# Performance work log

Measured on AMD Instinct MI355X. Metric: run time of the kernel, lower is better.

Reference implementation:

```python
import jax, jax.numpy as jnp
import numpy as np

N_SRC, N_DST, K, T = 16384, 8192, 16, 2
NODE_IN, EDGE_IN, TIME_D = 128, 64, 128
D_MODEL = NODE_IN + TIME_D + EDGE_IN  # 320
N_HEAD, D_K = 8, 64                   # d_k = d_v
HID = 128
LN_EPS = 1e-5


def setup_inputs() -> dict:
    key = jax.random.key(0)
    ks = jax.random.split(key, 10)
    std_qk = np.sqrt(2.0 / (D_MODEL + D_K)).astype(np.float32)
    return {
        "node_features": jax.random.normal(ks[0], (N_SRC, NODE_IN), jnp.float32),
        "edge_features": jax.random.normal(ks[1], (N_DST, K, T, EDGE_IN), jnp.float32),
        "delta_t": jax.random.uniform(ks[2], (N_DST, K, T), jnp.float32) * 100.0,
        "neigh_idx": jax.random.randint(ks[3], (N_DST, K), 0, N_SRC),
        "basis_freq": jnp.asarray(1.0 / 10 ** np.linspace(0, 9, TIME_D), jnp.float32),
        "phase": jnp.zeros((TIME_D,), jnp.float32),
        "w_qs": jax.random.normal(ks[4], (N_HEAD * D_K, D_MODEL), jnp.float32) * std_qk,
        "w_ks": jax.random.normal(ks[5], (N_HEAD * D_K, D_MODEL), jnp.float32) * std_qk,
        "w_vs": jax.random.normal(ks[6], (N_HEAD * D_K, D_MODEL), jnp.float32) * std_qk,
        "fc_w": jax.random.normal(ks[7], (D_MODEL, N_HEAD * D_K), jnp.float32) * 0.03,
        "fc_b": jnp.zeros((D_MODEL,), jnp.float32),
        "ln_g": jnp.ones((D_MODEL,), jnp.float32),
        "ln_b": jnp.zeros((D_MODEL,), jnp.float32),
        "node_w": jax.random.normal(ks[8], (HID, 2 * NODE_IN + TIME_D + EDGE_IN), jnp.float32) * 0.05,
        "node_b": jnp.zeros((HID,), jnp.float32),
    }


def reference(node_features, edge_features, delta_t, neigh_idx, basis_freq, phase,
              w_qs, w_ks, w_vs, fc_w, fc_b, ln_g, ln_b, node_w, node_b):
    h_dst = node_features[:N_DST]                                  # [N, NODE_IN]
    # message_func: per-edge time encoding + gather src feats + concat
    te = jnp.cos(delta_t[..., None] * basis_freq + phase)          # [N, K, T, TIME_D]
    h_nb = node_features[neigh_idx]                                # [N, K, NODE_IN] (irregular gather)
    h_nb = jnp.broadcast_to(h_nb[:, :, None, :], (N_DST, K, T, NODE_IN))
    m = jnp.concatenate([h_nb, edge_features, te], axis=-1)        # [N, K, T, D_MODEL]
    m = m.reshape(N_DST, K * T, D_MODEL)                           # mailbox kv
    # reduce_func query: [h_dst, zeros(edge_in), time_encode(0)=cos(phase)]
    t0 = jnp.broadcast_to(jnp.cos(phase), (N_DST, TIME_D))
    q = jnp.concatenate([h_dst, jnp.zeros((N_DST, EDGE_IN), h_dst.dtype), t0], axis=-1)  # [N, D_MODEL]
    # multi-head attention (len_q = 1)
    qh = (q @ w_qs.T).reshape(N_DST, N_HEAD, D_K)
    kh = (m @ w_ks.T).reshape(N_DST, K * T, N_HEAD, D_K)
    vh = (m @ w_vs.T).reshape(N_DST, K * T, N_HEAD, D_K)
    scores = jnp.einsum('nhd,nlhd->nhl', qh, kh) / np.float32(np.sqrt(D_K))
    attn = jax.nn.softmax(scores, axis=-1)
    ctx = jnp.einsum('nhl,nlhd->nhd', attn, vh).reshape(N_DST, N_HEAD * D_K)
    out = ctx @ fc_w.T + fc_b
    x = out + q                                                    # residual
    mu = x.mean(-1, keepdims=True)
    var = x.var(-1, keepdims=True)
    h_neigh = ln_g * (x - mu) * jax.lax.rsqrt(var + LN_EPS) + ln_b  # layer norm
    h = jnp.concatenate([h_dst, h_neigh], axis=-1)                 # [N, 2*NODE_IN+TIME_D+EDGE_IN]
    return jax.nn.relu(h @ node_w.T + node_b)                      # [N, HID]
```

## Files before the change

### kernel.cpp

```cpp
#include <hip/hip_runtime.h>
#include <math.h>

#define LNB      32
#define NODE_IN  128
#define EDGE_IN  64
#define TIME_D   128
#define D_MODEL  320
#define N_HEAD   8
#define D_K      64
#define NHD      512
#define HID      128
#define IN2      448
#define N_DSTN   8192

typedef __attribute__((ext_vector_type(8))) short bf16x8;
typedef __attribute__((ext_vector_type(4))) float f32x4;
#define MFMA16(a,b,c) __builtin_amdgcn_mfma_f32_16x16x32_bf16(a,b,c,0,0,0)

#define WS_QKM   0
#define WS_WQK   20971520
#define WS_WVF   21299200
#define WS_NWC   22118400
#define WS_F32   22175744
#define WS_X     22182784

#define F_C0     0
#define F_C0K    512
#define F_CC     3072
#define F_B2     3392

__device__ __forceinline__ unsigned short f2bf(float f) {
  __bf16 h = (__bf16)f;
  return __builtin_bit_cast(unsigned short, h);
}
__device__ __forceinline__ bf16x8 pack8(const float* v) {
  unsigned short b8[8];
  #pragma unroll
  for (int j = 0; j < 8; ++j) b8[j] = f2bf(v[j]);
  return *(const bf16x8*)b8;
}

#define GLDS(srcp, dstp) __builtin_amdgcn_global_load_lds(                     \
    (const __attribute__((address_space(1))) unsigned int*)(const void*)(srcp),\
    (__attribute__((address_space(3))) unsigned int*)(void*)(dstp), 16, 0, 0)

__global__ __launch_bounds__(256)
void prep1a(const float* __restrict__ nw, const float* __restrict__ lng,
            const float* __restrict__ fcb, const float* __restrict__ ph,
            unsigned short* __restrict__ ws)
{
  int i = blockIdx.x * 256 + threadIdx.x;
  unsigned short* nwc = ws + WS_NWC;
  float* f32r = (float*)(ws + WS_F32);
  if (i < 16384) {
    int o = i >> 7, k = i & 127;
    nwc[o * IN2 + k] = f2bf(nw[(size_t)o * IN2 + k]);
  } else if (i < 57344) {
    int j = i - 16384, o = j / 320, c = j - o * 320;
    nwc[o * IN2 + 128 + c] = f2bf(nw[(size_t)o * IN2 + 128 + c] * lng[c]);
  } else if (i < 57664) {
    int c = i - 57344;
    f32r[F_CC + c] = fcb[c] + (c >= 192 ? __cosf(ph[c - 192]) : 0.f);
  }
}

__global__ __launch_bounds__(256)
void prep1b(const float* __restrict__ wq, const float* __restrict__ ph,
            const float* __restrict__ nw, const float* __restrict__ lnb_,
            const float* __restrict__ nb, unsigned short* __restrict__ ws)
{
  float* f32r = (float*)(ws + WS_F32);
  int gw = (blockIdx.x * 256 + threadIdx.x) >> 6;
  int ln = threadIdx.x & 63;
  if (gw < 512) {
    float s = __cosf(ph[ln])      * wq[(size_t)gw * D_MODEL + 192 + ln]
            + __cosf(ph[ln + 64]) * wq[(size_t)gw * D_MODEL + 256 + ln];
    #pragma unroll
    for (int off = 32; off >= 1; off >>= 1) s += __shfl_xor(s, off);
    if (ln == 0) f32r[F_C0 + gw] = s;
  } else {
    int o = gw - 512;
    float s = 0.f;
    #pragma unroll
    for (int k = 0; k < 5; ++k) {
      int c = ln + 64 * k;
      s += nw[(size_t)o * IN2 + 128 + c] * lnb_[c];
    }
    #pragma unroll
    for (int off = 32; off >= 1; off >>= 1) s += __shfl_xor(s, off);
    if (ln == 0) f32r[F_B2 + o] = nb[o] + s;
  }
}

__global__ __launch_bounds__(256)
void prep_c0k(const float* __restrict__ wk, unsigned short* __restrict__ ws)
{
  float* f32r = (float*)(ws + WS_F32);
  int gw = (blockIdx.x * 256 + threadIdx.x) >> 6;
  int ln = threadIdx.x & 63;
  int h = gw / 320, d = gw - h * 320;
  float s = f32r[F_C0 + h * 64 + ln] * wk[(size_t)(h * 64 + ln) * D_MODEL + d];
  #pragma unroll
  for (int off = 32; off >= 1; off >>= 1) s += __shfl_xor(s, off);
  if (ln == 0) f32r[F_C0K + gw] = s;
}

__global__ __launch_bounds__(256)
void prep_wqk(const float* __restrict__ wq, const float* __restrict__ wk,
              unsigned short* __restrict__ ws)
{
  __shared__ float sQw[64 * 128];
  __shared__ float sKw[64 * 32];
  int h = blockIdx.x / 10, d0 = (blockIdx.x - h * 10) * 32;
  int tid = threadIdx.x;
  #pragma unroll 4
  for (int it = 0; it < 32; ++it) {
    int idx = it * 256 + tid;
    int r = idx >> 7, c = idx & 127;
    sQw[idx] = wq[(size_t)(h * 64 + r) * D_MODEL + c];
  }
  #pragma unroll
  for (int it = 0; it < 8; ++it) {
    int idx = it * 256 + tid;
    int r = idx >> 5, c = idx & 31;
    sKw[idx] = wk[(size_t)(h * 64 + r) * D_MODEL + d0 + c];
  }
  __syncthreads();
  int di = tid >> 3, k0 = (tid & 7) * 16;
  float acc[16] = {};
  for (int dk = 0; dk < 64; ++dk) {
    float w = sKw[dk * 32 + di];
    #pragma unroll
    for (int j = 0; j < 16; ++j) acc[j] += w * sQw[dk * 128 + k0 + j];
  }
  unsigned short* dst = ws + WS_WQK + (size_t)(h * 320 + d0 + di) * 128 + k0;
  #pragma unroll
  for (int j = 0; j < 16; ++j) dst[j] = f2bf(acc[j]);
}

__global__ __launch_bounds__(256)
void prep_wvf(const float* __restrict__ fcw, const float* __restrict__ wv,
              unsigned short* __restrict__ ws)
{
  __shared__ float sF[32 * 64];
  __shared__ float sW[64 * 32];
  int b = blockIdx.x;
  int h = b / 100, r2 = b - h * 100;
  int ct = r2 / 10;
  int c0 = ct * 32, d0 = (r2 - ct * 10) * 32;
  int tid = threadIdx.x;
  #pragma unroll
  for (int it = 0; it < 8; ++it) {
    int idx = it * 256 + tid;
    int i = idx >> 6, jj = idx & 63;
    sF[idx] = fcw[(size_t)(c0 + i) * NHD + h * 64 + jj];
  }
  #pragma unroll
  for (int it = 0; it < 8; ++it) {
    int idx = it * 256 + tid;
    int jj = idx >> 5, i = idx & 31;
    sW[idx] = wv[(size_t)(h * 64 + jj) * D_MODEL + d0 + i];
  }
  __syncthreads();
  int ci = tid >> 3, dj0 = (tid & 7) * 4;
  float acc[4] = {};
  for (int jj = 0; jj < 64; ++jj) {
    float f = sF[ci * 64 + jj];
    #pragma unroll
    for (int k = 0; k < 4; ++k) acc[k] += f * sW[jj * 32 + dj0 + k];
  }
  unsigned short* wvf = ws + WS_WVF;
  #pragma unroll
  for (int k = 0; k < 4; ++k)
    wvf[(size_t)(c0 + ci) * 2560 + (size_t)(d0 + dj0 + k) * 8 + h] = f2bf(acc[k]);
}

__global__ __launch_bounds__(256, 6)
void tgat_qk(const float* __restrict__ nf, const unsigned short* __restrict__ ws,
             unsigned short* __restrict__ qkm)
{
  __shared__ alignas(16) unsigned short sA[64 * 136];
  const int tid = threadIdx.x, wid = tid >> 6, lane = tid & 63, qd = lane >> 4, lm = lane & 15;
  const int mt_blk = blockIdx.x / 20, nt_blk = blockIdx.x - mt_blk * 20;
  const int n0 = mt_blk * 64, c0 = nt_blk * 128;
  const unsigned short* wqk = ws + WS_WQK;
  const float* f32r = (const float*)(ws + WS_F32);

  {
    int n = tid >> 2, k0 = (tid & 3) * 32;
    const float4* src = (const float4*)(nf + (size_t)(n0 + n) * NODE_IN + k0);
    #pragma unroll
    for (int q = 0; q < 4; ++q) {
      float4 f0 = src[2 * q], f1 = src[2 * q + 1];
      float v[8] = {f0.x, f0.y, f0.z, f0.w, f1.x, f1.y, f1.z, f1.w};
      *(bf16x8*)&sA[n * 136 + k0 + q * 8] = pack8(v);
    }
  }
  __syncthreads();

  f32x4 acc[2][4] = {};
  for (int kt = 0; kt < 4; ++kt) {
    bf16x8 a[4];
    #pragma unroll
    for (int mt = 0; mt < 4; ++mt)
      a[mt] = *(const bf16x8*)&sA[(mt * 16 + lm) * 136 + kt * 32 + qd * 8];
    #pragma unroll
    for (int t = 0; t < 2; ++t) {
      int cg = c0 + (2 * wid + t) * 16 + lm;
      bf16x8 b = *(const bf16x8*)&wqk[(size_t)cg * 128 + kt * 32 + qd * 8];
      #pragma unroll
      for (int mt = 0; mt < 4; ++mt) acc[t][mt] = MFMA16(a[mt], b, acc[t][mt]);
    }
  }
  #pragma unroll
  for (int t = 0; t < 2; ++t) {
    int cg = c0 + (2 * wid + t) * 16 + lm;
    float ck = f32r[F_C0K + cg];
    #pragma unroll
    for (int mt = 0; mt < 4; ++mt)
      #pragma unroll
      for (int r = 0; r < 4; ++r)
        qkm[(size_t)(n0 + mt * 16 + qd * 4 + r) * 2560 + cg] = f2bf(acc[t][mt][r] + ck);
  }
}

__global__ __launch_bounds__(256, 6)
void tgat_attn(const float* __restrict__ nf, const float* __restrict__ ef,
               const float* __restrict__ dtp, const int* __restrict__ nidx,
               const float* __restrict__ freq, const float* __restrict__ ph,
               unsigned short* __restrict__ qkm)
{
  __shared__ alignas(16) unsigned short sM[LNB * 328];
  __shared__ alignas(16) unsigned short sATT[16 * 40];

  const int tid = threadIdx.x;
  const int wid = tid >> 6, lane = tid & 63, qd = lane >> 4, lm = lane & 15;
  const int n = blockIdx.x;
  unsigned short* qn = qkm + (size_t)n * 2560;

  #pragma unroll 1
  for (int it = 0; it < 5; ++it) {
    int g = it * 256 + tid;
    int l = g & 31, dg = g >> 5;
    int d0 = dg * 8;
    float v[8];
    if (dg < 16) {
      int ni = nidx[n * 16 + (l >> 1)];
      const float4* src = (const float4*)(nf + (size_t)ni * NODE_IN + d0);
      float4 f0 = src[0], f1 = src[1];
      v[0]=f0.x; v[1]=f0.y; v[2]=f0.z; v[3]=f0.w; v[4]=f1.x; v[5]=f1.y; v[6]=f1.z; v[7]=f1.w;
    } else if (dg < 24) {
      const float4* src = (const float4*)(ef + ((size_t)n * LNB + l) * EDGE_IN + (d0 - NODE_IN));
      float4 f0 = src[0], f1 = src[1];
      v[0]=f0.x; v[1]=f0.y; v[2]=f0.z; v[3]=f0.w; v[4]=f1.x; v[5]=f1.y; v[6]=f1.z; v[7]=f1.w;
    } else {
      int dd = d0 - 192;
      float dt = dtp[(size_t)n * LNB + l];
      const float4* fq = (const float4*)(freq + dd);
      const float4* pp = (const float4*)(ph + dd);
      float4 q0 = fq[0], q1 = fq[1], p0 = pp[0], p1 = pp[1];
      v[0] = __cosf(dt * q0.x + p0.x); v[1] = __cosf(dt * q0.y + p0.y);
      v[2] = __cosf(dt * q0.z + p0.z); v[3] = __cosf(dt * q0.w + p0.w);
      v[4] = __cosf(dt * q1.x + p1.x); v[5] = __cosf(dt * q1.y + p1.y);
      v[6] = __cosf(dt * q1.z + p1.z); v[7] = __cosf(dt * q1.w + p1.w);
    }
    *(bf16x8*)&sM[l * 328 + d0] = pack8(v);
  }

  bf16x8 qfrag[10];
  if (wid == 0) {
    #pragma unroll
    for (int kt = 0; kt < 10; ++kt) {
      qfrag[kt] = (bf16x8){0,0,0,0,0,0,0,0};
      if (lm < 8) qfrag[kt] = *(const bf16x8*)&qn[lm * 320 + kt * 32 + qd * 8];
    }
  }
  __syncthreads();

  const int tbeg = (wid == 0) ? 0 : 2 + (wid - 1) * 6;
  const int tcnt = (wid == 0) ? 2 : 6;
  bf16x8 afr[6];

  if (wid == 0) {
    f32x4 acc0 = {}, acc1 = {};
    #pragma unroll
    for (int kt = 0; kt < 10; ++kt) {
      bf16x8 a0 = *(const bf16x8*)&sM[lm * 328 + kt * 32 + qd * 8];
      bf16x8 a1 = *(const bf16x8*)&sM[(16 + lm) * 328 + kt * 32 + qd * 8];
      acc0 = MFMA16(a0, qfrag[kt], acc0);
      acc1 = MFMA16(a1, qfrag[kt], acc1);
    }
    float s[8], e[8];
    #pragma unroll
    for (int r = 0; r < 4; ++r) { s[r] = acc0[r] * 0.125f; s[4 + r] = acc1[r] * 0.125f; }
    float mx = s[0];
    #pragma unroll
    for (int i = 1; i < 8; ++i) mx = fmaxf(mx, s[i]);
    mx = fmaxf(mx, __shfl_xor(mx, 16));
    mx = fmaxf(mx, __shfl_xor(mx, 32));
    float sum = 0.f;
    #pragma unroll
    for (int i = 0; i < 8; ++i) { e[i] = __expf(s[i] - mx); sum += e[i]; }
    sum += __shfl_xor(sum, 16);
    sum += __shfl_xor(sum, 32);
    float inv = 1.f / sum;
    #pragma unroll
    for (int i = 0; i < 8; ++i) {
      int l = (i < 4) ? (qd * 4 + i) : (16 + qd * 4 + (i - 4));
      sATT[lm * 40 + l] = f2bf(e[i] * inv);
    }
  } else {
    #pragma unroll
    for (int u = 0; u < 6; ++u) {
      int d = (tbeg + u) * 16 + lm;
      unsigned short a8[8];
      #pragma unroll
      for (int j = 0; j < 8; ++j) a8[j] = sM[(qd * 8 + j) * 328 + d];
      afr[u] = *(const bf16x8*)a8;
    }
  }
  __syncthreads();

  if (wid == 0) {
    #pragma unroll
    for (int u = 0; u < 2; ++u) {
      int d = u * 16 + lm;
      unsigned short a8[8];
      #pragma unroll
      for (int j = 0; j < 8; ++j) a8[j] = sM[(qd * 8 + j) * 328 + d];
      afr[u] = *(const bf16x8*)a8;
    }
  }
  bf16x8 batt = *(const bf16x8*)&sATT[lm * 40 + qd * 8];
  #pragma unroll
  for (int u = 0; u < 6; ++u) {
    if (u < tcnt) {
      int dtile = tbeg + u;
      f32x4 acc = {};
      acc = MFMA16(afr[u], batt, acc);
      if (lm < 8) {
        #pragma unroll
        for (int r = 0; r < 4; ++r)
          qn[(dtile * 16 + qd * 4 + r) * 8 + lm] = f2bf(acc[r]);
      }
    }
  }
}

__global__ __launch_bounds__(512, 1)
void tgat_xgemm(const unsigned short* __restrict__ ws,
                const unsigned short* __restrict__ qkm, float* __restrict__ xacc)
{
  __shared__ alignas(16) unsigned short sA[2][128 * 128];
  __shared__ alignas(16) unsigned short sB[2][80 * 128];
  const int tid = threadIdx.x, wid = tid >> 6, lane = tid & 63;
  const int qd = lane >> 4, lm = lane & 15;
  const int xcd = blockIdx.x & 7, j = blockIdx.x >> 3;
  const int nb = j & 3, mb = xcd + 8 * (j >> 2);
  const int n0 = mb * 128, c0 = nb * 80;
  const unsigned short* wvf = ws + WS_WVF;

  const int rhi = lane >> 4, blo = lane & 15;

  #define STAGE(kc, buf) {                                                     \
    for (int ri = wid; ri < 52; ri += 8) {                                     \
      if (ri < 32) {                                                           \
        int r = ri * 4 + rhi;                                                  \
        int blk = blo ^ (r & 7);                                               \
        GLDS(qkm + (size_t)(n0 + r) * 2560 + (kc) * 128 + blk * 8,             \
             &sA[buf][ri * 512]);                                              \
      } else {                                                                 \
        int jb = ri - 32;                                                      \
        int r = jb * 4 + rhi;                                                  \
        int blk = blo ^ (r & 7);                                               \
        GLDS(wvf + (size_t)(c0 + r) * 2560 + (kc) * 128 + blk * 8,             \
             &sB[buf][jb * 512]);                                              \
      }                                                                        \
    } }

  f32x4 acc[5] = {};
  STAGE(0, 0);
  __syncthreads();

  for (int c = 0; c < 20; ++c) {
    if (c < 19) STAGE(c + 1, (c + 1) & 1);
    const unsigned short* Ab = sA[c & 1];
    const unsigned short* Bb = sB[c & 1];
    const int s = lm & 7;
    #pragma unroll
    for (int kt = 0; kt < 4; ++kt) {
      const int blk = ((kt << 2) | qd) ^ s;
      bf16x8 a = *(const bf16x8*)&Ab[(wid * 16 + lm) * 128 + blk * 8];
      #pragma unroll
      for (int u = 0; u < 5; ++u) {
        bf16x8 b = *(const bf16x8*)&Bb[(u * 16 + lm) * 128 + blk * 8];
        acc[u] = MFMA16(a, b, acc[u]);
      }
    }
    __syncthreads();
  }

  #pragma unroll
  for (int u = 0; u < 5; ++u)
    #pragma unroll
    for (int r = 0; r < 4; ++r)
      xacc[(size_t)(n0 + wid * 16 + qd * 4 + r) * 320 + c0 + u * 16 + lm] = acc[u][r];
  #undef STAGE
}

__global__ __launch_bounds__(256, 4)
void tgat_post2(const float* __restrict__ nf, const unsigned short* __restrict__ ws,
                const float* __restrict__ xacc, float* __restrict__ out)
{
  __shared__ alignas(16) unsigned short sQb[16 * 136];
  __shared__ alignas(16) unsigned short sXb[16 * 328];
  const int tid = threadIdx.x, wid = tid >> 6, lane = tid & 63, qd = lane >> 4, lm = lane & 15;
  const int n0 = blockIdx.x * 16;
  const unsigned short* nwc = ws + WS_NWC;
  const float* f32r = (const float*)(ws + WS_F32);

  {
    int nn = tid >> 4, kk = (tid & 15) * 8;
    const float4* src = (const float4*)(nf + (size_t)(n0 + nn) * NODE_IN + kk);
    float4 f0 = src[0], f1 = src[1];
    float v8[8] = {f0.x, f0.y, f0.z, f0.w, f1.x, f1.y, f1.z, f1.w};
    *(bf16x8*)&sQb[nn * 136 + kk] = pack8(v8);
  }
  const int rr = tid >> 4, cl = tid & 15;
  float v[20], s1 = 0.f, s2 = 0.f;
  #pragma unroll
  for (int u = 0; u < 20; ++u) {
    int c = u * 16 + cl;
    float x = xacc[(size_t)(n0 + rr) * 320 + c] + f32r[F_CC + c];
    if (c < 128) x += nf[(size_t)(n0 + rr) * NODE_IN + c];
    v[u] = x; s1 += x; s2 += x * x;
  }
  #pragma unroll
  for (int off = 8; off >= 1; off >>= 1) { s1 += __shfl_xor(s1, off); s2 += __shfl_xor(s2, off); }
  float mean = s1 * (1.f / D_MODEL);
  float var  = s2 * (1.f / D_MODEL) - mean * mean;
  float rstd = rsqrtf(var + 1e-5f);
  #pragma unroll
  for (int u = 0; u < 20; ++u) {
    int c = u * 16 + cl;
    sXb[rr * 328 + c] = f2bf((v[u] - mean) * rstd);
  }
  __syncthreads();

  #pragma unroll
  for (int t = 0; t < 2; ++t) {
    int o = (wid * 2 + t) * 16 + lm;
    f32x4 acc = {};
    for (int kt = 0; kt < 14; ++kt) {
      bf16x8 a;
      if (kt < 4) a = *(const bf16x8*)&sQb[lm * 136 + kt * 32 + qd * 8];
      else        a = *(const bf16x8*)&sXb[lm * 328 + (kt - 4) * 32 + qd * 8];
      bf16x8 b = *(const bf16x8*)&nwc[(size_t)o * IN2 + kt * 32 + qd * 8];
      acc = MFMA16(a, b, acc);
    }
    float bz = f32r[F_B2 + o];
    #pragma unroll
    for (int r = 0; r < 4; ++r)
      out[(size_t)(n0 + qd * 4 + r) * HID + o] = fmaxf(acc[r] + bz, 0.f);
  }
}

extern "C" void kernel_launch(void* const* d_in, const int* in_sizes, int n_in,
                              void* d_out, int out_size, void* d_ws, size_t ws_size,
                              hipStream_t stream) {
  const float* nf   = (const float*)d_in[0];
  const float* ef   = (const float*)d_in[1];
  const float* dtp  = (const float*)d_in[2];
  const int*   nidx = (const int*)  d_in[3];
  const float* freq = (const float*)d_in[4];
  const float* ph   = (const float*)d_in[5];
  const float* wq   = (const float*)d_in[6];
  const float* wk   = (const float*)d_in[7];
  const float* wv   = (const float*)d_in[8];
  const float* fcw  = (const float*)d_in[9];
  const float* fcb  = (const float*)d_in[10];
  const float* lng  = (const float*)d_in[11];
  const float* lnb_ = (const float*)d_in[12];
  const float* nw   = (const float*)d_in[13];
  const float* nb   = (const float*)d_in[14];
  float* out = (float*)d_out;
  unsigned short* ws = (unsigned short*)d_ws;
  unsigned short* qkm = ws + WS_QKM;
  float* xacc = (float*)(ws + WS_X);

  prep1a  <<<226, 256, 0, stream>>>(nw, lng, fcb, ph, ws);
  prep1b  <<<160, 256, 0, stream>>>(wq, ph, nw, lnb_, nb, ws);
  prep_c0k<<<640, 256, 0, stream>>>(wk, ws);
  prep_wqk<<<80,  256, 0, stream>>>(wq, wk, ws);
  prep_wvf<<<800, 256, 0, stream>>>(fcw, wv, ws);
  tgat_qk   <<<2560, 256, 0, stream>>>(nf, ws, qkm);
  tgat_attn <<<8192, 256, 0, stream>>>(nf, ef, dtp, nidx, freq, ph, qkm);
  tgat_xgemm<<<256,  512, 0, stream>>>(ws, qkm, xacc);
  tgat_post2<<<512,  256, 0, stream>>>(nf, ws, xacc, out);
}
```

Measured before the change: 253.8 us.

## Merge prep kernels and overlap attention scoring with mailbox staging

Four weight-preparation kernels are merged into one launch that dispatches on block index, cutting launch overhead and serialization gaps. In the attention kernel, wave 0 now computes the scores by loading gathered features, edge features and time encodings straight from global memory into MFMA fragments. Meanwhile the other three waves fill the shared mailbox tile, so scoring and softmax no longer wait on a block-wide barrier. The final attention-times-V tiles are redistributed evenly across all four waves. Occupancy is lowered to 5 blocks per SIMD, and wave 0 now duplicates global loads.

```diff
diff --git a/kernel.cpp b/kernel.cpp
--- a/kernel.cpp
+++ b/kernel.cpp
@@ -45,50 +45,110 @@
     (__attribute__((address_space(3))) unsigned int*)(void*)(dstp), 16, 0, 0)
 
 __global__ __launch_bounds__(256)
-void prep1a(const float* __restrict__ nw, const float* __restrict__ lng,
-            const float* __restrict__ fcb, const float* __restrict__ ph,
-            unsigned short* __restrict__ ws)
+void prep_all(const float* __restrict__ nw, const float* __restrict__ lng,
+              const float* __restrict__ fcb, const float* __restrict__ ph,
+              const float* __restrict__ wq, const float* __restrict__ lnb_,
+              const float* __restrict__ nb, const float* __restrict__ wk,
+              const float* __restrict__ fcw, const float* __restrict__ wv,
+              unsigned short* __restrict__ ws)
 {
-  int i = blockIdx.x * 256 + threadIdx.x;
+  __shared__ float smem[10240];
+  const int b = blockIdx.x, tid = threadIdx.x;
   unsigned short* nwc = ws + WS_NWC;
   float* f32r = (float*)(ws + WS_F32);
-  if (i < 16384) {
-    int o = i >> 7, k = i & 127;
-    nwc[o * IN2 + k] = f2bf(nw[(size_t)o * IN2 + k]);
-  } else if (i < 57344) {
-    int j = i - 16384, o = j / 320, c = j - o * 320;
-    nwc[o * IN2 + 128 + c] = f2bf(nw[(size_t)o * IN2 + 128 + c] * lng[c]);
-  } else if (i < 57664) {
-    int c = i - 57344;
-    f32r[F_CC + c] = fcb[c] + (c >= 192 ? __cosf(ph[c - 192]) : 0.f);
-  }
-}
-
-__global__ __launch_bounds__(256)
-void prep1b(const float* __restrict__ wq, const float* __restrict__ ph,
-            const float* __restrict__ nw, const float* __restrict__ lnb_,
-            const float* __restrict__ nb, unsigned short* __restrict__ ws)
-{
-  float* f32r = (float*)(ws + WS_F32);
-  int gw = (blockIdx.x * 256 + threadIdx.x) >> 6;
-  int ln = threadIdx.x & 63;
-  if (gw < 512) {
-    float s = __cosf(ph[ln])      * wq[(size_t)gw * D_MODEL + 192 + ln]
-            + __cosf(ph[ln + 64]) * wq[(size_t)gw * D_MODEL + 256 + ln];
-    #pragma unroll
-    for (int off = 32; off >= 1; off >>= 1) s += __shfl_xor(s, off);
-    if (ln == 0) f32r[F_C0 + gw] = s;
+
+  if (b < 226) {
+    int i = b * 256 + tid;
+    if (i < 16384) {
+      int o = i >> 7, k = i & 127;
+      nwc[o * IN2 + k] = f2bf(nw[(size_t)o * IN2 + k]);
+    } else if (i < 57344) {
+      int j = i - 16384, o = j / 320, c = j - o * 320;
+      nwc[o * IN2 + 128 + c] = f2bf(nw[(size_t)o * IN2 + 128 + c] * lng[c]);
+    } else if (i < 57664) {
+      int c = i - 57344;
+      f32r[F_CC + c] = fcb[c] + (c >= 192 ? __cosf(ph[c - 192]) : 0.f);
+    }
+  } else if (b < 386) {
+    int gw = ((b - 226) * 256 + tid) >> 6;
+    int ln = tid & 63;
+    if (gw < 512) {
+      float s = __cosf(ph[ln])      * wq[(size_t)gw * D_MODEL + 192 + ln]
+              + __cosf(ph[ln + 64]) * wq[(size_t)gw * D_MODEL + 256 + ln];
+      #pragma unroll
+      for (int off = 32; off >= 1; off >>= 1) s += __shfl_xor(s, off);
+      if (ln == 0) f32r[F_C0 + gw] = s;
+    } else {
+      int o = gw - 512;
+      float s = 0.f;
+      #pragma unroll
+      for (int k = 0; k < 5; ++k) {
+        int c = ln + 64 * k;
+        s += nw[(size_t)o * IN2 + 128 + c] * lnb_[c];
+      }
+      #pragma unroll
+      for (int off = 32; off >= 1; off >>= 1) s += __shfl_xor(s, off);
+      if (ln == 0) f32r[F_B2 + o] = nb[o] + s;
+    }
+  } else if (b < 466) {
+    float* sQw = smem;
+    float* sKw = smem + 8192;
+    int bw = b - 386;
+    int h = bw / 10, d0 = (bw - h * 10) * 32;
+    #pragma unroll 4
+    for (int it = 0; it < 32; ++it) {
+      int idx = it * 256 + tid;
+      int r = idx >> 7, c = idx & 127;
+      sQw[idx] = wq[(size_t)(h * 64 + r) * D_MODEL + c];
+    }
+    #pragma unroll
+    for (int it = 0; it < 8; ++it) {
+      int idx = it * 256 + tid;
+      int r = idx >> 5, c = idx & 31;
+      sKw[idx] = wk[(size_t)(h * 64 + r) * D_MODEL + d0 + c];
+    }
+    __syncthreads();
+    int di = tid >> 3, k0 = (tid & 7) * 16;
+    float acc[16] = {};
+    for (int dk = 0; dk < 64; ++dk) {
+      float w = sKw[dk * 32 + di];
+      #pragma unroll
+      for (int j = 0; j < 16; ++j) acc[j] += w * sQw[dk * 128 + k0 + j];
+    }
+    unsigned short* dst = ws + WS_WQK + (size_t)(h * 320 + d0 + di) * 128 + k0;
+    #pragma unroll
+    for (int j = 0; j < 16; ++j) dst[j] = f2bf(acc[j]);
   } else {
-    int o = gw - 512;
-    float s = 0.f;
-    #pragma unroll
-    for (int k = 0; k < 5; ++k) {
-      int c = ln + 64 * k;
-      s += nw[(size_t)o * IN2 + 128 + c] * lnb_[c];
-    }
-    #pragma unroll
-    for (int off = 32; off >= 1; off >>= 1) s += __shfl_xor(s, off);
-    if (ln == 0) f32r[F_B2 + o] = nb[o] + s;
+    float* sF = smem;
+    float* sW = smem + 2048;
+    int bb = b - 466;
+    int h = bb / 100, r2 = bb - h * 100;
+    int ct = r2 / 10;
+    int c0 = ct * 32, d0 = (r2 - ct * 10) * 32;
+    #pragma unroll
+    for (int it = 0; it < 8; ++it) {
+      int idx = it * 256 + tid;
+      int i = idx >> 6, jj = idx & 63;
+      sF[idx] = fcw[(size_t)(c0 + i) * NHD + h * 64 + jj];
+    }
+    #pragma unroll
+    for (int it = 0; it < 8; ++it) {
+      int idx = it * 256 + tid;
+      int jj = idx >> 5, i = idx & 31;
+      sW[idx] = wv[(size_t)(h * 64 + jj) * D_MODEL + d0 + i];
+    }
+    __syncthreads();
+    int ci = tid >> 3, dj0 = (tid & 7) * 4;
+    float acc[4] = {};
+    for (int jj = 0; jj < 64; ++jj) {
+      float f = sF[ci * 64 + jj];
+      #pragma unroll
+      for (int k = 0; k < 4; ++k) acc[k] += f * sW[jj * 32 + dj0 + k];
+    }
+    unsigned short* wvf = ws + WS_WVF;
+    #pragma unroll
+    for (int k = 0; k < 4; ++k)
+      wvf[(size_t)(c0 + ci) * 2560 + (size_t)(d0 + dj0 + k) * 8 + h] = f2bf(acc[k]);
   }
 }
 
@@ -103,76 +163,6 @@
   #pragma unroll
   for (int off = 32; off >= 1; off >>= 1) s += __shfl_xor(s, off);
   if (ln == 0) f32r[F_C0K + gw] = s;
-}
-
-__global__ __launch_bounds__(256)
-void prep_wqk(const float* __restrict__ wq, const float* __restrict__ wk,
-              unsigned short* __restrict__ ws)
-{
-  __shared__ float sQw[64 * 128];
-  __shared__ float sKw[64 * 32];
-  int h = blockIdx.x / 10, d0 = (blockIdx.x - h * 10) * 32;
-  int tid = threadIdx.x;
-  #pragma unroll 4
-  for (int it = 0; it < 32; ++it) {
-    int idx = it * 256 + tid;
-    int r = idx >> 7, c = idx & 127;
-    sQw[idx] = wq[(size_t)(h * 64 + r) * D_MODEL + c];
-  }
-  #pragma unroll
-  for (int it = 0; it < 8; ++it) {
-    int idx = it * 256 + tid;
-    int r = idx >> 5, c = idx & 31;
-    sKw[idx] = wk[(size_t)(h * 64 + r) * D_MODEL + d0 + c];
-  }
-  __syncthreads();
-  int di = tid >> 3, k0 = (tid & 7) * 16;
-  float acc[16] = {};
-  for (int dk = 0; dk < 64; ++dk) {
-    float w = sKw[dk * 32 + di];
-    #pragma unroll
-    for (int j = 0; j < 16; ++j) acc[j] += w * sQw[dk * 128 + k0 + j];
-  }
-  unsigned short* dst = ws + WS_WQK + (size_t)(h * 320 + d0 + di) * 128 + k0;
-  #pragma unroll
-  for (int j = 0; j < 16; ++j) dst[j] = f2bf(acc[j]);
-}
-
-__global__ __launch_bounds__(256)
-void prep_wvf(const float* __restrict__ fcw, const float* __restrict__ wv,
-              unsigned short* __restrict__ ws)
-{
-  __shared__ float sF[32 * 64];
-  __shared__ float sW[64 * 32];
-  int b = blockIdx.x;
-  int h = b / 100, r2 = b - h * 100;
-  int ct = r2 / 10;
-  int c0 = ct * 32, d0 = (r2 - ct * 10) * 32;
-  int tid = threadIdx.x;
-  #pragma unroll
-  for (int it = 0; it < 8; ++it) {
-    int idx = it * 256 + tid;
-    int i = idx >> 6, jj = idx & 63;
-    sF[idx] = fcw[(size_t)(c0 + i) * NHD + h * 64 + jj];
-  }
-  #pragma unroll
-  for (int it = 0; it < 8; ++it) {
-    int idx = it * 256 + tid;
-    int jj = idx >> 5, i = idx & 31;
-    sW[idx] = wv[(size_t)(h * 64 + jj) * D_MODEL + d0 + i];
-  }
-  __syncthreads();
-  int ci = tid >> 3, dj0 = (tid & 7) * 4;
-  float acc[4] = {};
-  for (int jj = 0; jj < 64; ++jj) {
-    float f = sF[ci * 64 + jj];
-    #pragma unroll
-    for (int k = 0; k < 4; ++k) acc[k] += f * sW[jj * 32 + dj0 + k];
-  }
-  unsigned short* wvf = ws + WS_WVF;
-  #pragma unroll
-  for (int k = 0; k < 4; ++k)
-    wvf[(size_t)(c0 + ci) * 2560 + (size_t)(d0 + dj0 + k) * 8 + h] = f2bf(acc[k]);
 }
 
 __global__ __launch_bounds__(256, 6)
@@ -224,7 +214,7 @@
   }
 }
 
-__global__ __launch_bounds__(256, 6)
+__global__ __launch_bounds__(256, 5)
 void tgat_attn(const float* __restrict__ nf, const float* __restrict__ ef,
                const float* __restrict__ dtp, const int* __restrict__ nidx,
                const float* __restrict__ freq, const float* __restrict__ ph,
@@ -238,57 +228,56 @@
   const int n = blockIdx.x;
   unsigned short* qn = qkm + (size_t)n * 2560;
 
-  #pragma unroll 1
-  for (int it = 0; it < 5; ++it) {
-    int g = it * 256 + tid;
-    int l = g & 31, dg = g >> 5;
-    int d0 = dg * 8;
-    float v[8];
-    if (dg < 16) {
-      int ni = nidx[n * 16 + (l >> 1)];
-      const float4* src = (const float4*)(nf + (size_t)ni * NODE_IN + d0);
-      float4 f0 = src[0], f1 = src[1];
-      v[0]=f0.x; v[1]=f0.y; v[2]=f0.z; v[3]=f0.w; v[4]=f1.x; v[5]=f1.y; v[6]=f1.z; v[7]=f1.w;
-    } else if (dg < 24) {
-      const float4* src = (const float4*)(ef + ((size_t)n * LNB + l) * EDGE_IN + (d0 - NODE_IN));
-      float4 f0 = src[0], f1 = src[1];
-      v[0]=f0.x; v[1]=f0.y; v[2]=f0.z; v[3]=f0.w; v[4]=f1.x; v[5]=f1.y; v[6]=f1.z; v[7]=f1.w;
-    } else {
-      int dd = d0 - 192;
-      float dt = dtp[(size_t)n * LNB + l];
+  if (wid == 0) {
+    const int ni0 = nidx[n * 16 + (lm >> 1)];
+    const int ni1 = nidx[n * 16 + 8 + (lm >> 1)];
+    const float dt0 = dtp[(size_t)n * LNB + lm];
+    const float dt1 = dtp[(size_t)n * LNB + 16 + lm];
+    f32x4 acc0 = {}, acc1 = {};
+    #pragma unroll
+    for (int kt = 0; kt < 4; ++kt) {
+      bf16x8 qf = (bf16x8){0,0,0,0,0,0,0,0};
+      if (lm < 8) qf = *(const bf16x8*)&qn[lm * 320 + kt * 32 + qd * 8];
+      const int d0 = kt * 32 + qd * 8;
+      const float4* s0 = (const float4*)(nf + (size_t)ni0 * NODE_IN + d0);
+      const float4* s1 = (const float4*)(nf + (size_t)ni1 * NODE_IN + d0);
+      float4 a = s0[0], b = s0[1], c = s1[0], d = s1[1];
+      float v0[8] = {a.x,a.y,a.z,a.w,b.x,b.y,b.z,b.w};
+      float v1[8] = {c.x,c.y,c.z,c.w,d.x,d.y,d.z,d.w};
+      acc0 = MFMA16(pack8(v0), qf, acc0);
+      acc1 = MFMA16(pack8(v1), qf, acc1);
+    }
+    #pragma unroll
+    for (int kt = 4; kt < 6; ++kt) {
+      bf16x8 qf = (bf16x8){0,0,0,0,0,0,0,0};
+      if (lm < 8) qf = *(const bf16x8*)&qn[lm * 320 + kt * 32 + qd * 8];
+      const int e0 = kt * 32 + qd * 8 - 128;
+      const float4* s0 = (const float4*)(ef + ((size_t)n * LNB + lm) * EDGE_IN + e0);
+      const float4* s1 = (const float4*)(ef + ((size_t)n * LNB + 16 + lm) * EDGE_IN + e0);
+      float4 a = s0[0], b = s0[1], c = s1[0], d = s1[1];
+      float v0[8] = {a.x,a.y,a.z,a.w,b.x,b.y,b.z,b.w};
+      float v1[8] = {c.x,c.y,c.z,c.w,d.x,d.y,d.z,d.w};
+      acc0 = MFMA16(pack8(v0), qf, acc0);
+      acc1 = MFMA16(pack8(v1), qf, acc1);
+    }
+    #pragma unroll
+    for (int kt = 6; kt < 10; ++kt) {
+      bf16x8 qf = (bf16x8){0,0,0,0,0,0,0,0};
+      if (lm < 8) qf = *(const bf16x8*)&qn[lm * 320 + kt * 32 + qd * 8];
+      const int dd = kt * 32 + qd * 8 - 192;
       const float4* fq = (const float4*)(freq + dd);
       const float4* pp = (const float4*)(ph + dd);
-      float4 q0 = fq[0], q1 = fq[1], p0 = pp[0], p1 = pp[1];
-      v[0] = __cosf(dt * q0.x + p0.x); v[1] = __cosf(dt * q0.y + p0.y);
-      v[2] = __cosf(dt * q0.z + p0.z); v[3] = __cosf(dt * q0.w + p0.w);
-      v[4] = __cosf(dt * q1.x + p1.x); v[5] = __cosf(dt * q1.y + p1.y);
-      v[6] = __cosf(dt * q1.z + p1.z); v[7] = __cosf(dt * q1.w + p1.w);
-    }
-    *(bf16x8*)&sM[l * 328 + d0] = pack8(v);
-  }
-
-  bf16x8 qfrag[10];
-  if (wid == 0) {
-    #pragma unroll
-    for (int kt = 0; kt < 10; ++kt) {
-      qfrag[kt] = (bf16x8){0,0,0,0,0,0,0,0};
-      if (lm < 8) qfrag[kt] = *(const bf16x8*)&qn[lm * 320 + kt * 32 + qd * 8];
-    }
-  }
-  __syncthreads();
-
-  const int tbeg = (wid == 0) ? 0 : 2 + (wid - 1) * 6;
-  const int tcnt = (wid == 0) ? 2 : 6;
-  bf16x8 afr[6];
-
-  if (wid == 0) {
-    f32x4 acc0 = {}, acc1 = {};
-    #pragma unroll
-    for (int kt = 0; kt < 10; ++kt) {
-      bf16x8 a0 = *(const bf16x8*)&sM[lm * 328 + kt * 32 + qd * 8];
-      bf16x8 a1 = *(const bf16x8*)&sM[(16 + lm) * 328 + kt * 32 + qd * 8];
-      acc0 = MFMA16(a0, qfrag[kt], acc0);
-      acc1 = MFMA16(a1, qfrag[kt], acc1);
+      float4 f0 = fq[0], f1 = fq[1], p0 = pp[0], p1 = pp[1];
+      float v0[8] = {__cosf(dt0*f0.x+p0.x), __cosf(dt0*f0.y+p0.y),
+                     __cosf(dt0*f0.z+p0.z), __cosf(dt0*f0.w+p0.w),
+                     __cosf(dt0*f1.x+p1.x), __cosf(dt0*f1.y+p1.y),
+                     __cosf(dt0*f1.z+p1.z), __cosf(dt0*f1.w+p1.w)};
+      float v1[8] = {__cosf(dt1*f0.x+p0.x), __cosf(dt1*f0.y+p0.y),
+                     __cosf(dt1*f0.z+p0.z), __cosf(dt1*f0.w+p0.w),
+                     __cosf(dt1*f1.x+p1.x), __cosf(dt1*f1.y+p1.y),
+                     __cosf(dt1*f1.z+p1.z), __cosf(dt1*f1.w+p1.w)};
+      acc0 = MFMA16(pack8(v0), qf, acc0);
+      acc1 = MFMA16(pack8(v1), qf, acc1);
     }
     float s[8], e[8];
     #pragma unroll
@@ -310,39 +299,54 @@
       sATT[lm * 40 + l] = f2bf(e[i] * inv);
     }
   } else {
-    #pragma unroll
-    for (int u = 0; u < 6; ++u) {
-      int d = (tbeg + u) * 16 + lm;
-      unsigned short a8[8];
-      #pragma unroll
-      for (int j = 0; j < 8; ++j) a8[j] = sM[(qd * 8 + j) * 328 + d];
-      afr[u] = *(const bf16x8*)a8;
+    const int t3 = tid - 64;
+    #pragma unroll 1
+    for (int it = 0; it < 7; ++it) {
+      int g = it * 192 + t3;
+      if (g < 1280) {
+        int l = g & 31, dg = g >> 5;
+        int d0 = dg * 8;
+        float v[8];
+        if (dg < 16) {
+          int ni = nidx[n * 16 + (l >> 1)];
+          const float4* src = (const float4*)(nf + (size_t)ni * NODE_IN + d0);
+          float4 f0 = src[0], f1 = src[1];
+          v[0]=f0.x; v[1]=f0.y; v[2]=f0.z; v[3]=f0.w; v[4]=f1.x; v[5]=f1.y; v[6]=f1.z; v[7]=f1.w;
+        } else if (dg < 24) {
+          const float4* src = (const float4*)(ef + ((size_t)n * LNB + l) * EDGE_IN + (d0 - NODE_IN));
+          float4 f0 = src[0], f1 = src[1];
+          v[0]=f0.x; v[1]=f0.y; v[2]=f0.z; v[3]=f0.w; v[4]=f1.x; v[5]=f1.y; v[6]=f1.z; v[7]=f1.w;
+        } else {
+          int dd = d0 - 192;
+          float dt = dtp[(size_t)n * LNB + l];
+          const float4* fq = (const float4*)(freq + dd);
+          const float4* pp = (const float4*)(ph + dd);
+          float4 q0 = fq[0], q1 = fq[1], p0 = pp[0], p1 = pp[1];
+          v[0] = __cosf(dt * q0.x + p0.x); v[1] = __cosf(dt * q0.y + p0.y);
+          v[2] = __cosf(dt * q0.z + p0.z); v[3] = __cosf(dt * q0.w + p0.w);
+          v[4] = __cosf(dt * q1.x + p1.x); v[5] = __cosf(dt * q1.y + p1.y);
+          v[6] = __cosf(dt * q1.z + p1.z); v[7] = __cosf(dt * q1.w + p1.w);
+        }
+        *(bf16x8*)&sM[l * 328 + d0] = pack8(v);
+      }
     }
   }
   __syncthreads();
 
-  if (wid == 0) {
-    #pragma unroll
-    for (int u = 0; u < 2; ++u) {
-      int d = u * 16 + lm;
-      unsigned short a8[8];
-      #pragma unroll
-      for (int j = 0; j < 8; ++j) a8[j] = sM[(qd * 8 + j) * 328 + d];
-      afr[u] = *(const bf16x8*)a8;
-    }
-  }
   bf16x8 batt = *(const bf16x8*)&sATT[lm * 40 + qd * 8];
   #pragma unroll
-  for (int u = 0; u < 6; ++u) {
-    if (u < tcnt) {
-      int dtile = tbeg + u;
-      f32x4 acc = {};
-      acc = MFMA16(afr[u], batt, acc);
-      if (lm < 8) {
-        #pragma unroll
-        for (int r = 0; r < 4; ++r)
-          qn[(dtile * 16 + qd * 4 + r) * 8 + lm] = f2bf(acc[r]);
-      }
+  for (int u = 0; u < 5; ++u) {
+    const int dtile = wid * 5 + u;
+    const int d = dtile * 16 + lm;
+    unsigned short a8[8];
+    #pragma unroll
+    for (int j = 0; j < 8; ++j) a8[j] = sM[(qd * 8 + j) * 328 + d];
+    f32x4 acc = {};
+    acc = MFMA16(*(const bf16x8*)a8, batt, acc);
+    if (lm < 8) {
+      #pragma unroll
+      for (int r = 0; r < 4; ++r)
+        qn[(dtile * 16 + qd * 4 + r) * 8 + lm] = f2bf(acc[r]);
     }
   }
 }
@@ -488,11 +492,8 @@
   unsigned short* qkm = ws + WS_QKM;
   float* xacc = (float*)(ws + WS_X);
 
-  prep1a  <<<226, 256, 0, stream>>>(nw, lng, fcb, ph, ws);
-  prep1b  <<<160, 256, 0, stream>>>(wq, ph, nw, lnb_, nb, ws);
+  prep_all<<<1266, 256, 0, stream>>>(nw, lng, fcb, ph, wq, lnb_, nb, wk, fcw, wv, ws);
   prep_c0k<<<640, 256, 0, stream>>>(wk, ws);
-  prep_wqk<<<80,  256, 0, stream>>>(wq, wk, ws);
-  prep_wvf<<<800, 256, 0, stream>>>(fcw, wv, ws);
   tgat_qk   <<<2560, 256, 0, stream>>>(nf, ws, qkm);
   tgat_attn <<<8192, 256, 0, stream>>>(nf, ef, dtp, nidx, freq, ph, qkm);
   tgat_xgemm<<<256,  512, 0, stream>>>(ws, qkm, xacc);
```

Result: slower. 261.5 us (+3.0%).
